# Kernel optimization log

Measured on AMD Instinct MI355X. Metric: run time of the kernel, lower is better.

Reference implementation:

```python
import jax, jax.numpy as jnp
import numpy as np

NR_HEADS = 8


def segment_softmax(scores, indices, num_segments):
    # numerically stable softmax within each segment
    seg_max = jax.ops.segment_max(scores, indices, num_segments=num_segments)
    e = jnp.exp(scores - seg_max[indices])
    denom = jax.ops.segment_sum(e, indices, num_segments=num_segments)
    return e / denom[indices]


def setup_inputs() -> dict:
    key = jax.random.key(0)
    ks = jax.random.split(key, 10)
    n_ast, d, n_cfg = 500000, 128, 32768
    H, combined = NR_HEADS, 128
    w_scale = 1.0 / np.sqrt(d)
    return {
        "ast_nodes_encodings": jax.random.normal(ks[0], (n_ast, d), jnp.float32),
        "Wq": jax.random.normal(ks[1], (H, d, d), jnp.float32) * w_scale,
        "bq": jnp.zeros((H, d), jnp.float32),
        "Wk": jax.random.normal(ks[2], (H, d, d), jnp.float32) * w_scale,
        "bk": jnp.zeros((H, d), jnp.float32),
        "Wo": jax.random.normal(ks[3], (H * d, combined), jnp.float32) * (1.0 / np.sqrt(H * d)),
        "bo": jnp.zeros((combined,), jnp.float32),
        "ast_key": jax.random.randint(ks[4], (n_ast,), 0, n_ast, jnp.int32),
        "ast_value": jax.random.randint(ks[5], (n_ast,), 0, n_cfg, jnp.int32),
        "pdg_key": jnp.arange(n_cfg, dtype=jnp.int32),
        "pdg_value": jax.random.randint(ks[6], (n_cfg,), 0, n_ast, jnp.int32),
        "nr_cfg_nodes": n_cfg,
    }


def reference(ast_nodes_encodings, Wq, bq, Wk, bk, Wo, bo,
              ast_key, ast_value, pdg_key, pdg_value, nr_cfg_nodes):
    N = int(nr_cfg_nodes)
    d = ast_nodes_encodings.shape[1]
    inv_sqrt_d = 1.0 / np.sqrt(d)

    # Build per-PDG-node attention queries: gather sub-AST root encodings, scatter into [N, d]
    root_encodings = ast_nodes_encodings[pdg_value]                   # [N_map, d]
    attn_queries = jnp.zeros((N, d), ast_nodes_encodings.dtype).at[pdg_key].set(root_encodings)

    # Gather scattered inputs (one row per AST node assigned to a PDG node)
    values = ast_nodes_encodings[ast_key]                              # [E, d]
    indices = ast_value                                                # [E]

    # Multi-head scatter attention (ScatterCombiner with combining_method='attn')
    head_outs = []
    for h in range(NR_HEADS):  # small fixed head count; avoids [E, H, d] intermediates
        q = attn_queries @ Wq[h] + bq[h]                               # [N, d]
        k = values @ Wk[h] + bk[h]                                     # [E, d]
        scores = jnp.sum(q[indices] * k, axis=-1) * inv_sqrt_d         # [E]
        probs = segment_softmax(scores, indices, N)                    # [E]
        head_outs.append(jax.ops.segment_sum(probs[:, None] * values, indices, num_segments=N))

    combined = jnp.concatenate(head_outs, axis=-1) @ Wo + bo           # [N, combined_dim]
    return combined
```

## Files before the change

### kernel.cpp

```cpp
#include <hip/hip_runtime.h>
#include <hip/hip_bf16.h>
#include <cstdint>

typedef __hip_bfloat16 bf16;
typedef unsigned int uint;
typedef unsigned short ushort;

#define DEVI __device__ __forceinline__

DEVI float blo(uint u){ return __uint_as_float(u << 16); }
DEVI float bhi(uint u){ return __uint_as_float(u & 0xffff0000u); }
DEVI ushort f2b(float x){ uint u = __float_as_uint(x); uint r = (u + 0x7fffu + ((u >> 16) & 1u)) >> 16; return (ushort)r; }
DEVI uint pack2(float a, float b){ return (uint)f2b(a) | ((uint)f2b(b) << 16); }
DEVI float b2f(ushort h){ return __uint_as_float((uint)h << 16); }

typedef short bf16x8 __attribute__((ext_vector_type(8)));
typedef float f32x4  __attribute__((ext_vector_type(4)));

DEVI float row16_sum(float x){
  int y;
  y = __builtin_amdgcn_update_dpp(0, __float_as_int(x), 0x121, 0xF, 0xF, true); x += __int_as_float(y);
  y = __builtin_amdgcn_update_dpp(0, __float_as_int(x), 0x122, 0xF, 0xF, true); x += __int_as_float(y);
  y = __builtin_amdgcn_update_dpp(0, __float_as_int(x), 0x124, 0xF, 0xF, true); x += __int_as_float(y);
  y = __builtin_amdgcn_update_dpp(0, __float_as_int(x), 0x128, 0xF, 0xF, true); x += __int_as_float(y);
  return x;
}

DEVI void frag_pack_body(const float* __restrict__ S, uint4* __restrict__ D, int C, int ctn, int b, int l){
  const int ks = b / ctn, ct = b - ks*ctn;
  const int kb = ks*32 + (l >> 4)*8;
  const int c  = ct*16 + (l & 15);
  ushort hi[8], lo[8];
  #pragma unroll
  for (int j = 0; j < 8; ++j){
    float wv = S[(size_t)(kb + j)*C + c];
    ushort hh = f2b(wv);
    hi[j] = hh;
    lo[j] = f2b(wv - b2f(hh));
  }
  uint4 H, L;
  H.x = (uint)hi[0] | ((uint)hi[1] << 16);
  H.y = (uint)hi[2] | ((uint)hi[3] << 16);
  H.z = (uint)hi[4] | ((uint)hi[5] << 16);
  H.w = (uint)hi[6] | ((uint)hi[7] << 16);
  L.x = (uint)lo[0] | ((uint)lo[1] << 16);
  L.y = (uint)lo[2] | ((uint)lo[3] << 16);
  L.z = (uint)lo[4] | ((uint)lo[5] << 16);
  L.w = (uint)lo[6] | ((uint)lo[7] << 16);
  D[((size_t)b*2 + 0)*64 + l] = H;
  D[((size_t)b*2 + 1)*64 + l] = L;
}

__global__ __launch_bounds__(256) void prep1(
    const float* __restrict__ Wq, const float* __restrict__ Wk,
    const float* __restrict__ bq, const float* __restrict__ bk,
    const float* __restrict__ Wo, const int* __restrict__ av,
    float* __restrict__ Mb, float* __restrict__ cvec, float* __restrict__ uvec,
    float* __restrict__ sv, uint4* __restrict__ Wp, int* __restrict__ counts, int E)
{
  __shared__ float WkL[128*33];
  __shared__ float WqL[16*33];
  const int b = blockIdx.x, t = threadIdx.x;
  if (b < 64){
    const int h = b >> 3, pg = b & 7, p0 = pg*16;
    const float* wk = Wk + (size_t)h*16384;
    const float* wq = Wq + ((size_t)h*128 + p0)*128;
    const int m = t & 127, half = t >> 7;
    float acc[8] = {0,0,0,0,0,0,0,0};
    for (int jc = 0; jc < 4; ++jc){
      __syncthreads();
      #pragma unroll
      for (int i = 0; i < 4; ++i){
        int g = t + 256*i;
        int mm = g >> 3, j0 = (g & 7)*4;
        float4 v = *(const float4*)(wk + mm*128 + jc*32 + j0);
        float* d = &WkL[mm*33 + j0];
        d[0] = v.x; d[1] = v.y; d[2] = v.z; d[3] = v.w;
      }
      {
        int e = t*2;
        int pr = e >> 5, jj = e & 31;
        float2 v = *(const float2*)(wq + pr*128 + jc*32 + jj);
        WqL[pr*33 + jj] = v.x; WqL[pr*33 + jj + 1] = v.y;
      }
      __syncthreads();
      for (int j = 0; j < 32; ++j){
        float wkv = WkL[m*33 + j];
        #pragma unroll
        for (int r = 0; r < 8; ++r)
          acc[r] = fmaf(WqL[(half*8 + r)*33 + j], wkv, acc[r]);
      }
    }
    #pragma unroll
    for (int r = 0; r < 8; ++r)
      Mb[(size_t)(p0 + half*8 + r)*1024 + h*128 + m] = acc[r];
  } else if (b < 72){
    if (t < 128){
      int h = b - 64, m = t;
      const float* wkr = Wk + ((size_t)h*128 + m)*128;
      const float* wqr = Wq + ((size_t)h*128 + m)*128;
      const float* bqr = bq + h*128;
      const float* bkr = bk + h*128;
      float c = 0.f, u = 0.f;
      for (int j = 0; j < 128; ++j){
        c = fmaf(wkr[j], bqr[j], c);
        u = fmaf(wqr[j], bkr[j], u);
      }
      cvec[h*128 + m] = c;
      uvec[h*128 + m] = u;
      if (m == 0){
        float s = 0.f;
        for (int j = 0; j < 128; ++j) s = fmaf(bqr[j], bkr[j], s);
        sv[h] = s;
      }
    }
  } else if (b < 328){
    if (t < 64) frag_pack_body(Wo, Wp, 128, 8, b - 72, t);
  } else {
    int e = (b - 328)*256 + t;
    if (e < E) atomicAdd(&counts[av[e]], 1);
  }
}

__global__ __launch_bounds__(256) void prep2(
    const int* __restrict__ counts, int* __restrict__ offsets, int N,
    const float* __restrict__ Mb, uint4* __restrict__ Mp,
    const int* __restrict__ pk, const int* __restrict__ pv,
    const float* __restrict__ ast, float* __restrict__ aq,
    ushort* __restrict__ aqh, ushort* __restrict__ aql, int n_map)
{
  __shared__ int pa[256];
  __shared__ int pb[256];
  const int b = blockIdx.x, t = threadIdx.x;
  if (b == 0){
    const int CH = (N + 255) >> 8;
    int b0 = t*CH, e0 = b0 + CH;
    if (b0 > N) b0 = N;
    if (e0 > N) e0 = N;
    int s = 0;
    for (int i = b0; i < e0; ++i) s += counts[i];
    pa[t] = s;
    __syncthreads();
    int* src = pa; int* dst = pb;
    for (int off = 1; off < 256; off <<= 1){
      int v = src[t];
      if (t >= off) v += src[t - off];
      __syncthreads();
      dst[t] = v;
      __syncthreads();
      int* tmp = src; src = dst; dst = tmp;
    }
    int run = src[t] - s;
    for (int i = b0; i < e0; ++i){ offsets[i] = run; run += counts[i]; }
    if (t == 255) offsets[N] = src[255];
  } else if (b < 257){
    if (t < 64) frag_pack_body(Mb, Mp, 1024, 64, b - 1, t);
  } else {
    int i = (b - 257)*4 + (t >> 6);
    int lane = t & 63;
    if (i < n_map){
      int k = pk[i], src = pv[i];
      float2 v = *(const float2*)(ast + (size_t)src*128 + 2*lane);
      *(float2*)(aq + (size_t)k*128 + 2*lane) = v;
      ushort h0 = f2b(v.x), h1 = f2b(v.y);
      ushort l0 = f2b(v.x - b2f(h0)), l1 = f2b(v.y - b2f(h1));
      *(uint*)(aqh + (size_t)k*128 + 2*lane) = (uint)h0 | ((uint)h1 << 16);
      *(uint*)(aql + (size_t)k*128 + 2*lane) = (uint)l0 | ((uint)l1 << 16);
    }
  }
}

__global__ __launch_bounds__(256) void prep3(
    const float* __restrict__ aq, const float* __restrict__ uvec, const float* __restrict__ sv,
    float* __restrict__ qb, const int* __restrict__ av, const int* __restrict__ akey,
    const int* __restrict__ offsets, int* __restrict__ cursor, int* __restrict__ ridx,
    int N, int E)
{
  const int b = blockIdx.x, t = threadIdx.x;
  const int nqb = (N + 3) >> 2;
  if (b < nqb){
    int n = b*4 + (t >> 6);
    int lane = t & 63;
    if (n < N){
      int h = lane >> 3, g = lane & 7;
      const float* ar = aq + (size_t)n*128 + g*16;
      const float* ur = uvec + h*128 + g*16;
      float dot = 0.f;
      #pragma unroll
      for (int k = 0; k < 16; ++k) dot = fmaf(ar[k], ur[k], dot);
      dot += __shfl_xor(dot, 1);
      dot += __shfl_xor(dot, 2);
      dot += __shfl_xor(dot, 4);
      if (g == 0) qb[(size_t)n*8 + h] = dot + sv[h];
    }
  } else {
    int e = (b - nqb)*256 + t;
    if (e < E){
      int seg = av[e];
      int pos = offsets[seg] + atomicAdd(&cursor[seg], 1);
      ridx[pos] = akey[e];
    }
  }
}

__global__ __launch_bounds__(256, 1) void qt_mfma(const ushort* __restrict__ aqh, const ushort* __restrict__ aql,
                                                  const uint4* __restrict__ Mp, const float* __restrict__ cvec,
                                                  bf16* __restrict__ qt, int N){
  const int l = threadIdx.x & 63, w = threadIdx.x >> 6;
  const int lr = l & 15, lk = l >> 4;
  const int r0 = blockIdx.x*128 + w*32;
  int ra = r0 + lr;      if (ra > N-1) ra = N-1;
  int rb = r0 + 16 + lr; if (rb > N-1) rb = N-1;

  bf16x8 Ah0[4], Al0[4], Ah1[4], Al1[4];
  #pragma unroll
  for (int ks = 0; ks < 4; ++ks){
    Ah0[ks] = *(const bf16x8*)(aqh + (size_t)ra*128 + lk*8 + ks*32);
    Al0[ks] = *(const bf16x8*)(aql + (size_t)ra*128 + lk*8 + ks*32);
    Ah1[ks] = *(const bf16x8*)(aqh + (size_t)rb*128 + lk*8 + ks*32);
    Al1[ks] = *(const bf16x8*)(aql + (size_t)rb*128 + lk*8 + ks*32);
  }
  const uint4* pw = Mp + l;

  bf16x8 Ba[8], Bb[8];
  auto LDB = [&](int ct, bf16x8* B){
    #pragma unroll
    for (int ks = 0; ks < 4; ++ks){
      const uint4* q = pw + ((size_t)(ks*64 + ct)*2)*64;
      B[ks*2]   = *(const bf16x8*)q;
      B[ks*2+1] = *(const bf16x8*)(q + 64);
    }
  };
  auto DO = [&](int ct, bf16x8* B){
    f32x4 a0 = {0.f,0.f,0.f,0.f}, a1 = {0.f,0.f,0.f,0.f};
    #pragma unroll
    for (int ks = 0; ks < 4; ++ks){
      a0 = __builtin_amdgcn_mfma_f32_16x16x32_bf16(Ah0[ks], B[2*ks],   a0, 0, 0, 0);
      a1 = __builtin_amdgcn_mfma_f32_16x16x32_bf16(Ah1[ks], B[2*ks],   a1, 0, 0, 0);
      a0 = __builtin_amdgcn_mfma_f32_16x16x32_bf16(Al0[ks], B[2*ks],   a0, 0, 0, 0);
      a1 = __builtin_amdgcn_mfma_f32_16x16x32_bf16(Al1[ks], B[2*ks],   a1, 0, 0, 0);
      a0 = __builtin_amdgcn_mfma_f32_16x16x32_bf16(Ah0[ks], B[2*ks+1], a0, 0, 0, 0);
      a1 = __builtin_amdgcn_mfma_f32_16x16x32_bf16(Ah1[ks], B[2*ks+1], a1, 0, 0, 0);
    }
    const int cc = ct*16 + lr;
    const float bv = cvec[cc];
    #pragma unroll
    for (int i = 0; i < 4; ++i){
      int rr0 = r0 + lk*4 + i;
      if (rr0 < N) ((ushort*)qt)[(size_t)rr0*1024 + cc] = f2b(a0[i] + bv);
      int rr1 = r0 + 16 + lk*4 + i;
      if (rr1 < N) ((ushort*)qt)[(size_t)rr1*1024 + cc] = f2b(a1[i] + bv);
    }
  };

  LDB(0, Ba);
  for (int ct = 0; ct < 64; ct += 2){
    LDB(ct + 1, Bb);
    DO(ct, Ba);
    if (ct + 2 < 64) LDB(ct + 2, Ba);
    DO(ct + 1, Bb);
  }
}

__global__ __launch_bounds__(256, 4) void seg_attn(
    const bf16* __restrict__ qt, const float* __restrict__ qb,
    const int* __restrict__ offsets, const int* __restrict__ ridx,
    const float* __restrict__ ast, bf16* __restrict__ ho, int N)
{
  const int wid  = threadIdx.x >> 6;
  const int lane = threadIdx.x & 63;
  const int n = blockIdx.x*4 + wid;
  if (n >= N) return;
  const int beg = __builtin_amdgcn_readfirstlane(offsets[n]);
  const int end = __builtin_amdgcn_readfirstlane(offsets[n+1]);
  const int deg = end - beg;
  const int grp = lane >> 4, d4 = lane & 15;
  const int h0 = 2*grp, h1 = 2*grp + 1;

  const ushort* qtp = (const ushort*)qt + (size_t)n*1024 + d4*8;
  const uint4 Qa = *(const uint4*)(qtp + h0*128);
  const uint4 Qb = *(const uint4*)(qtp + h1*128);
  const float4 q0lo = make_float4(blo(Qa.x), bhi(Qa.x), blo(Qa.y), bhi(Qa.y));
  const float4 q0hi = make_float4(blo(Qa.z), bhi(Qa.z), blo(Qa.w), bhi(Qa.w));
  const float4 q1lo = make_float4(blo(Qb.x), bhi(Qb.x), blo(Qb.y), bhi(Qb.y));
  const float4 q1hi = make_float4(blo(Qb.z), bhi(Qb.z), blo(Qb.w), bhi(Qb.w));
  const float SC = 0.12751744886681336f;
  const float qs0 = qb[(size_t)n*8 + h0] * SC;
  const float qs1 = qb[(size_t)n*8 + h1] * SC;

  const int* rp = ridx + beg;

  float den0 = 0.f, den1 = 0.f;
  float4 x0lo = make_float4(0,0,0,0), x0hi = x0lo, x1lo = x0lo, x1hi = x0lo;

  if (deg > 0){
#define LOADP(Pa0, Pa1, Pb0, Pb1, base) do { \
    int iA = (base) < deg ? (base) : deg-1; \
    int iB = (base)+1 < deg ? (base)+1 : deg-1; \
    const float4* pA = (const float4*)(ast + (size_t)rp[iA]*128 + d4*8); \
    const float4* pB = (const float4*)(ast + (size_t)rp[iB]*128 + d4*8); \
    Pa0 = pA[0]; Pa1 = pA[1]; Pb0 = pB[0]; Pb1 = pB[1]; } while(0)

#define C1(A0, A1) do { \
    float s0, s1; \
    s0 = A0.x*q0lo.x; s0 = fmaf(A0.y, q0lo.y, s0); s0 = fmaf(A0.z, q0lo.z, s0); s0 = fmaf(A0.w, q0lo.w, s0); \
    s0 = fmaf(A1.x, q0hi.x, s0); s0 = fmaf(A1.y, q0hi.y, s0); s0 = fmaf(A1.z, q0hi.z, s0); s0 = fmaf(A1.w, q0hi.w, s0); \
    s1 = A0.x*q1lo.x; s1 = fmaf(A0.y, q1lo.y, s1); s1 = fmaf(A0.z, q1lo.z, s1); s1 = fmaf(A0.w, q1lo.w, s1); \
    s1 = fmaf(A1.x, q1hi.x, s1); s1 = fmaf(A1.y, q1hi.y, s1); s1 = fmaf(A1.z, q1hi.z, s1); s1 = fmaf(A1.w, q1hi.w, s1); \
    s0 = row16_sum(s0); s1 = row16_sum(s1); \
    const float p0 = exp2f(fmaf(s0, SC, qs0)); \
    const float p1 = exp2f(fmaf(s1, SC, qs1)); \
    den0 += p0; den1 += p1; \
    x0lo.x = fmaf(p0, A0.x, x0lo.x); x0lo.y = fmaf(p0, A0.y, x0lo.y); \
    x0lo.z = fmaf(p0, A0.z, x0lo.z); x0lo.w = fmaf(p0, A0.w, x0lo.w); \
    x0hi.x = fmaf(p0, A1.x, x0hi.x); x0hi.y = fmaf(p0, A1.y, x0hi.y); \
    x0hi.z = fmaf(p0, A1.z, x0hi.z); x0hi.w = fmaf(p0, A1.w, x0hi.w); \
    x1lo.x = fmaf(p1, A0.x, x1lo.x); x1lo.y = fmaf(p1, A0.y, x1lo.y); \
    x1lo.z = fmaf(p1, A0.z, x1lo.z); x1lo.w = fmaf(p1, A0.w, x1lo.w); \
    x1hi.x = fmaf(p1, A1.x, x1hi.x); x1hi.y = fmaf(p1, A1.y, x1hi.y); \
    x1hi.z = fmaf(p1, A1.z, x1hi.z); x1hi.w = fmaf(p1, A1.w, x1hi.w); \
  } while(0)

    float4 P0a0, P0a1, P0b0, P0b1;
    float4 P1a0, P1a1, P1b0, P1b1;
    float4 P2a0, P2a1, P2b0, P2b1;
    LOADP(P0a0, P0a1, P0b0, P0b1, 0);
    LOADP(P1a0, P1a1, P1b0, P1b1, 2);
    LOADP(P2a0, P2a1, P2b0, P2b1, 4);
    int e = 0;
    for (; e + 5 < deg; e += 6){
      C1(P0a0, P0a1); C1(P0b0, P0b1); LOADP(P0a0, P0a1, P0b0, P0b1, e + 6);
      C1(P1a0, P1a1); C1(P1b0, P1b1); LOADP(P1a0, P1a1, P1b0, P1b1, e + 8);
      C1(P2a0, P2a1); C1(P2b0, P2b1); LOADP(P2a0, P2a1, P2b0, P2b1, e + 10);
    }
    const int t = deg - e;
    if (t >= 1) C1(P0a0, P0a1);
    if (t >= 2) C1(P0b0, P0b1);
    if (t >= 3) C1(P1a0, P1a1);
    if (t >= 4) C1(P1b0, P1b1);
    if (t >= 5) C1(P2a0, P2a1);
    if (t >= 6) C1(P2b0, P2b1);
#undef C1
#undef LOADP
  }
  const float r0v = (deg > 0) ? (1.f / den0) : 0.f;
  const float r1v = (deg > 0) ? (1.f / den1) : 0.f;

  uint4 o0, o1;
  o0.x = pack2(x0lo.x*r0v, x0lo.y*r0v); o0.y = pack2(x0lo.z*r0v, x0lo.w*r0v);
  o0.z = pack2(x0hi.x*r0v, x0hi.y*r0v); o0.w = pack2(x0hi.z*r0v, x0hi.w*r0v);
  o1.x = pack2(x1lo.x*r1v, x1lo.y*r1v); o1.y = pack2(x1lo.z*r1v, x1lo.w*r1v);
  o1.z = pack2(x1hi.x*r1v, x1hi.y*r1v); o1.w = pack2(x1hi.z*r1v, x1hi.w*r1v);
  ushort* hb = (ushort*)ho + (size_t)n*1024 + d4*8;
  *(uint4*)(hb + h0*128) = o0;
  *(uint4*)(hb + h1*128) = o1;
}

__global__ __launch_bounds__(256, 1) void out_mfma(const bf16* __restrict__ ho, const uint4* __restrict__ Wp,
                                                   const float* __restrict__ bo, float* __restrict__ out, int N){
  const int l = threadIdx.x & 63, w = threadIdx.x >> 6;
  const int lr = l & 15, lk = l >> 4;
  const int r0 = blockIdx.x*128 + w*32;
  int ra = r0 + lr;      if (ra > N-1) ra = N-1;
  int rb = r0 + 16 + lr; if (rb > N-1) rb = N-1;
  const bf16* pa = ho + (size_t)ra*1024 + lk*8;
  const bf16* pb = ho + (size_t)rb*1024 + lk*8;
  const uint4* pw = Wp + l;

  f32x4 acc[2][8];
  #pragma unroll
  for (int i = 0; i < 2; ++i)
    #pragma unroll
    for (int c = 0; c < 8; ++c)
      #pragma unroll
      for (int j = 0; j < 4; ++j) acc[i][c][j] = 0.f;

  bf16x8 Aa[2], Ab[2], Ba[16], Bb[16];

  auto LD = [&](int ks, bf16x8* A, bf16x8* B){
    A[0] = *(const bf16x8*)(pa + ks*32);
    A[1] = *(const bf16x8*)(pb + ks*32);
    const uint4* q = pw + (size_t)ks*1024;
    #pragma unroll
    for (int u = 0; u < 16; ++u) B[u] = *(const bf16x8*)(q + (size_t)u*64);
  };
  auto MM = [&](bf16x8* A, bf16x8* B){
    #pragma unroll
    for (int c = 0; c < 8; ++c){
      acc[0][c] = __builtin_amdgcn_mfma_f32_16x16x32_bf16(A[0], B[2*c],   acc[0][c], 0, 0, 0);
      acc[1][c] = __builtin_amdgcn_mfma_f32_16x16x32_bf16(A[1], B[2*c],   acc[1][c], 0, 0, 0);
      acc[0][c] = __builtin_amdgcn_mfma_f32_16x16x32_bf16(A[0], B[2*c+1], acc[0][c], 0, 0, 0);
      acc[1][c] = __builtin_amdgcn_mfma_f32_16x16x32_bf16(A[1], B[2*c+1], acc[1][c], 0, 0, 0);
    }
  };

  LD(0, Aa, Ba);
  for (int ks = 0; ks < 32; ks += 2){
    LD(ks + 1, Ab, Bb);
    MM(Aa, Ba);
    if (ks + 2 < 32) LD(ks + 2, Aa, Ba);
    MM(Ab, Bb);
  }

  #pragma unroll
  for (int c = 0; c < 8; ++c){
    float bv = bo[c*16 + lr];
    #pragma unroll
    for (int rt = 0; rt < 2; ++rt){
      #pragma unroll
      for (int i = 0; i < 4; ++i){
        int rr = r0 + rt*16 + lk*4 + i;
        if (rr < N) out[(size_t)rr*128 + c*16 + lr] = acc[rt][c][i] + bv;
      }
    }
  }
}

extern "C" void kernel_launch(void* const* d_in, const int* in_sizes, int n_in,
                              void* d_out, int out_size, void* d_ws, size_t ws_size,
                              hipStream_t stream) {
  const float* ast = (const float*)d_in[0];
  const float* Wq  = (const float*)d_in[1];
  const float* bq  = (const float*)d_in[2];
  const float* Wk  = (const float*)d_in[3];
  const float* bk  = (const float*)d_in[4];
  const float* Wo  = (const float*)d_in[5];
  const float* bo  = (const float*)d_in[6];
  const int* ast_key   = (const int*)d_in[7];
  const int* ast_value = (const int*)d_in[8];
  const int* pdg_key   = (const int*)d_in[9];
  const int* pdg_value = (const int*)d_in[10];
  const int E     = in_sizes[7];
  const int n_map = in_sizes[9];
  const int N     = out_size / 128;
  float* out = (float*)d_out;

  char* w = (char*)d_ws;
  auto carve = [&](size_t bytes)->char*{
    char* p = w; w += (bytes + 255) & ~size_t(255); return p;
  };
  bf16*  qt      = (bf16*) carve((size_t)N*1024*2);
  float* aq      = (float*)carve((size_t)N*128*4);
  ushort* aqh    = (ushort*)carve((size_t)N*128*2);
  ushort* aql    = (ushort*)carve((size_t)N*128*2);
  float* Mb      = (float*)carve((size_t)128*1024*4);
  float* cvec    = (float*)carve(1024*4);
  float* uvec    = (float*)carve(1024*4);
  float* sv      = (float*)carve(8*4);
  float* qb      = (float*)carve((size_t)N*8*4);
  int*   counts  = (int*)  carve((size_t)N*4);
  int*   cursor  = (int*)  carve((size_t)N*4);
  int*   offsets = (int*)  carve((size_t)(N+1)*4);
  int*   ridx    = (int*)  carve((size_t)E*4);
  bf16*  ho      = (bf16*) carve((size_t)N*1024*2);
  uint4* Wp      = (uint4*)carve((size_t)256*2*64*16);
  uint4* Mp      = (uint4*)carve((size_t)256*2*64*16);
  (void)ws_size; (void)n_in;

  hipMemsetAsync(aq,     0, (size_t)N*128*8, stream);
  hipMemsetAsync(counts, 0, (size_t)N*8, stream);

  const int nb_cnt  = (E + 255)/256;
  const int nb_sca  = (n_map + 3)/4;
  const int nb_qb   = (N + 3)/4;

  prep1<<<328 + nb_cnt, 256, 0, stream>>>(Wq, Wk, bq, bk, Wo, ast_value, Mb, cvec, uvec, sv, Wp, counts, E);
  prep2<<<257 + nb_sca, 256, 0, stream>>>(counts, offsets, N, Mb, Mp, pdg_key, pdg_value, ast, aq, aqh, aql, n_map);
  qt_mfma<<<(N + 127)/128, 256, 0, stream>>>(aqh, aql, Mp, cvec, qt, N);
  prep3<<<nb_qb + nb_cnt, 256, 0, stream>>>(aq, uvec, sv, qb, ast_value, ast_key, offsets, cursor, ridx, N, E);
  seg_attn<<<(N + 3)/4, 256, 0, stream>>>(qt, qb, offsets, ridx, ast, ho, N);
  out_mfma<<<(N + 127)/128, 256, 0, stream>>>(ho, Wp, bo, out, N);
}
```

Baseline: 694.7 us.

## Process segments in descending-degree order and deepen seg_attn prefetch to eight rows

Builds a histogram of segment degrees, prefix-sums it in descending order, and counting-sorts node ids into a permutation so seg_attn schedules the heaviest segments first. This targets load imbalance and the long tail from Poisson-distributed segment sizes. It also raises the software-pipelined prefetch depth in the gather loop from six to eight rows, which uses more registers. Memset and kernel order are adjusted so the permutation is built before seg_attn, at the cost of extra small kernels' worth of work and an indirect perm lookup per wave.

```diff
diff --git a/kernel.cpp b/kernel.cpp
--- a/kernel.cpp
+++ b/kernel.cpp
@@ -127,7 +127,8 @@
     const float* __restrict__ Mb, uint4* __restrict__ Mp,
     const int* __restrict__ pk, const int* __restrict__ pv,
     const float* __restrict__ ast, float* __restrict__ aq,
-    ushort* __restrict__ aqh, ushort* __restrict__ aql, int n_map)
+    ushort* __restrict__ aqh, ushort* __restrict__ aql, int n_map,
+    int* __restrict__ hist, int nb_sca)
 {
   __shared__ int pa[256];
   __shared__ int pb[256];
@@ -155,7 +156,7 @@
     if (t == 255) offsets[N] = src[255];
   } else if (b < 257){
     if (t < 64) frag_pack_body(Mb, Mp, 1024, 64, b - 1, t);
-  } else {
+  } else if (b < 257 + nb_sca){
     int i = (b - 257)*4 + (t >> 6);
     int lane = t & 63;
     if (i < n_map){
@@ -167,6 +168,12 @@
       *(uint*)(aqh + (size_t)k*128 + 2*lane) = (uint)h0 | ((uint)h1 << 16);
       *(uint*)(aql + (size_t)k*128 + 2*lane) = (uint)l0 | ((uint)l1 << 16);
     }
+  } else {
+    int n = (b - 257 - nb_sca)*256 + t;
+    if (n < N){
+      int d = counts[n]; if (d > 1023) d = 1023;
+      atomicAdd(&hist[d], 1);
+    }
   }
 }
 
@@ -174,10 +181,13 @@
     const float* __restrict__ aq, const float* __restrict__ uvec, const float* __restrict__ sv,
     float* __restrict__ qb, const int* __restrict__ av, const int* __restrict__ akey,
     const int* __restrict__ offsets, int* __restrict__ cursor, int* __restrict__ ridx,
-    int N, int E)
+    int N, int E, const int* __restrict__ hist, int* __restrict__ hstart)
 {
+  __shared__ int pa[256];
+  __shared__ int pb[256];
   const int b = blockIdx.x, t = threadIdx.x;
   const int nqb = (N + 3) >> 2;
+  const int nbc = (E + 255) >> 8;
   if (b < nqb){
     int n = b*4 + (t >> 6);
     int lane = t & 63;
@@ -193,19 +203,53 @@
       dot += __shfl_xor(dot, 4);
       if (g == 0) qb[(size_t)n*8 + h] = dot + sv[h];
     }
-  } else {
+  } else if (b < nqb + nbc){
     int e = (b - nqb)*256 + t;
     if (e < E){
       int seg = av[e];
       int pos = offsets[seg] + atomicAdd(&cursor[seg], 1);
       ridx[pos] = akey[e];
     }
+  } else {
+    int s = 0;
+    const int base = t*4;
+    #pragma unroll
+    for (int j = 0; j < 4; ++j) s += hist[1023 - (base + j)];
+    pa[t] = s;
+    __syncthreads();
+    int* src = pa; int* dst = pb;
+    for (int off = 1; off < 256; off <<= 1){
+      int v = src[t];
+      if (t >= off) v += src[t - off];
+      __syncthreads();
+      dst[t] = v;
+      __syncthreads();
+      int* tmp = src; src = dst; dst = tmp;
+    }
+    int run = src[t] - s;
+    #pragma unroll
+    for (int j = 0; j < 4; ++j){
+      int d = 1023 - (base + j);
+      hstart[d] = run;
+      run += hist[d];
+    }
   }
 }
 
 __global__ __launch_bounds__(256, 1) void qt_mfma(const ushort* __restrict__ aqh, const ushort* __restrict__ aql,
                                                   const uint4* __restrict__ Mp, const float* __restrict__ cvec,
-                                                  bf16* __restrict__ qt, int N){
+                                                  bf16* __restrict__ qt, int N,
+                                                  const int* __restrict__ counts, const int* __restrict__ hstart,
+                                                  int* __restrict__ hcur, int* __restrict__ perm, int nbq){
+  if ((int)blockIdx.x >= nbq){
+    int n = ((int)blockIdx.x - nbq)*256 + (int)threadIdx.x;
+    if (n < N){
+      int d = counts[n]; if (d > 1023) d = 1023;
+      int pos = hstart[d] + atomicAdd(&hcur[d], 1);
+      perm[pos] = n;
+    }
+    return;
+  }
   const int l = threadIdx.x & 63, w = threadIdx.x >> 6;
   const int lr = l & 15, lk = l >> 4;
   const int r0 = blockIdx.x*128 + w*32;
@@ -265,12 +309,14 @@
 __global__ __launch_bounds__(256, 4) void seg_attn(
     const bf16* __restrict__ qt, const float* __restrict__ qb,
     const int* __restrict__ offsets, const int* __restrict__ ridx,
-    const float* __restrict__ ast, bf16* __restrict__ ho, int N)
+    const float* __restrict__ ast, bf16* __restrict__ ho,
+    const int* __restrict__ perm, int N)
 {
   const int wid  = threadIdx.x >> 6;
   const int lane = threadIdx.x & 63;
-  const int n = blockIdx.x*4 + wid;
-  if (n >= N) return;
+  const int slot = blockIdx.x*4 + wid;
+  if (slot >= N) return;
+  const int n = __builtin_amdgcn_readfirstlane(perm[slot]);
   const int beg = __builtin_amdgcn_readfirstlane(offsets[n]);
   const int end = __builtin_amdgcn_readfirstlane(offsets[n+1]);
   const int deg = end - beg;
@@ -324,14 +370,17 @@
     float4 P0a0, P0a1, P0b0, P0b1;
     float4 P1a0, P1a1, P1b0, P1b1;
     float4 P2a0, P2a1, P2b0, P2b1;
+    float4 P3a0, P3a1, P3b0, P3b1;
     LOADP(P0a0, P0a1, P0b0, P0b1, 0);
     LOADP(P1a0, P1a1, P1b0, P1b1, 2);
     LOADP(P2a0, P2a1, P2b0, P2b1, 4);
+    LOADP(P3a0, P3a1, P3b0, P3b1, 6);
     int e = 0;
-    for (; e + 5 < deg; e += 6){
-      C1(P0a0, P0a1); C1(P0b0, P0b1); LOADP(P0a0, P0a1, P0b0, P0b1, e + 6);
-      C1(P1a0, P1a1); C1(P1b0, P1b1); LOADP(P1a0, P1a1, P1b0, P1b1, e + 8);
-      C1(P2a0, P2a1); C1(P2b0, P2b1); LOADP(P2a0, P2a1, P2b0, P2b1, e + 10);
+    for (; e + 7 < deg; e += 8){
+      C1(P0a0, P0a1); C1(P0b0, P0b1); LOADP(P0a0, P0a1, P0b0, P0b1, e + 8);
+      C1(P1a0, P1a1); C1(P1b0, P1b1); LOADP(P1a0, P1a1, P1b0, P1b1, e + 10);
+      C1(P2a0, P2a1); C1(P2b0, P2b1); LOADP(P2a0, P2a1, P2b0, P2b1, e + 12);
+      C1(P3a0, P3a1); C1(P3b0, P3b1); LOADP(P3a0, P3a1, P3b0, P3b1, e + 14);
     }
     const int t = deg - e;
     if (t >= 1) C1(P0a0, P0a1);
@@ -340,6 +389,8 @@
     if (t >= 4) C1(P1b0, P1b1);
     if (t >= 5) C1(P2a0, P2a1);
     if (t >= 6) C1(P2b0, P2b1);
+    if (t >= 7) C1(P3a0, P3a1);
+    if (t >= 8) C1(P3b0, P3b1);
 #undef C1
 #undef LOADP
   }
@@ -450,24 +501,30 @@
   float* qb      = (float*)carve((size_t)N*8*4);
   int*   counts  = (int*)  carve((size_t)N*4);
   int*   cursor  = (int*)  carve((size_t)N*4);
+  int*   hist    = (int*)  carve(1024*4);
+  int*   hcur    = (int*)  carve(1024*4);
   int*   offsets = (int*)  carve((size_t)(N+1)*4);
   int*   ridx    = (int*)  carve((size_t)E*4);
+  int*   hstart  = (int*)  carve(1024*4);
+  int*   perm    = (int*)  carve((size_t)N*4);
   bf16*  ho      = (bf16*) carve((size_t)N*1024*2);
   uint4* Wp      = (uint4*)carve((size_t)256*2*64*16);
   uint4* Mp      = (uint4*)carve((size_t)256*2*64*16);
   (void)ws_size; (void)n_in;
 
   hipMemsetAsync(aq,     0, (size_t)N*128*8, stream);
-  hipMemsetAsync(counts, 0, (size_t)N*8, stream);
-
-  const int nb_cnt  = (E + 255)/256;
-  const int nb_sca  = (n_map + 3)/4;
-  const int nb_qb   = (N + 3)/4;
+  hipMemsetAsync(counts, 0, (size_t)N*8 + 8192, stream);
+
+  const int nb_cnt = (E + 255)/256;
+  const int nb_sca = (n_map + 3)/4;
+  const int nb_qb  = (N + 3)/4;
+  const int nb_seg = (N + 255)/256;
+  const int nbq    = (N + 127)/128;
 
   prep1<<<328 + nb_cnt, 256, 0, stream>>>(Wq, Wk, bq, bk, Wo, ast_value, Mb, cvec, uvec, sv, Wp, counts, E);
-  prep2<<<257 + nb_sca, 256, 0, stream>>>(counts, offsets, N, Mb, Mp, pdg_key, pdg_value, ast, aq, aqh, aql, n_map);
-  qt_mfma<<<(N + 127)/128, 256, 0, stream>>>(aqh, aql, Mp, cvec, qt, N);
-  prep3<<<nb_qb + nb_cnt, 256, 0, stream>>>(aq, uvec, sv, qb, ast_value, ast_key, offsets, cursor, ridx, N, E);
-  seg_attn<<<(N + 3)/4, 256, 0, stream>>>(qt, qb, offsets, ridx, ast, ho, N);
-  out_mfma<<<(N + 127)/128, 256, 0, stream>>>(ho, Wp, bo, out, N);
-}
+  prep2<<<257 + nb_sca + nb_seg, 256, 0, stream>>>(counts, offsets, N, Mb, Mp, pdg_key, pdg_value, ast, aq, aqh, aql, n_map, hist, nb_sca);
+  prep3<<<nb_qb + nb_cnt + 1, 256, 0, stream>>>(aq, uvec, sv, qb, ast_value, ast_key, offsets, cursor, ridx, N, E, hist, hstart);
+  qt_mfma<<<nbq + nb_seg, 256, 0, stream>>>(aqh, aql, Mp, cvec, qt, N, counts, hstart, hcur, perm, nbq);
+  seg_attn<<<(N + 3)/4, 256, 0, stream>>>(qt, qb, offsets, ridx, ast, ho, perm, N);
+  out_mfma<<<nbq, 256, 0, stream>>>(ho, Wp, bo, out, N);
+}
```

After: 1.024 ms. +47.4%, slower.
